# Kernel optimization log

Hardware: AMD Instinct MI355X
Metric: run time of the kernel (lower is better)

The kernel has to match this reference:

```python
import jax, jax.numpy as jnp
import numpy as np

B, C, L = 256, 256, 512
EPS = 1e-5

def setup_inputs() -> dict:
    key = jax.random.key(0)
    k1, k2, k3, k4 = jax.random.split(key, 4)
    x = jax.random.normal(k1, (B, C, L), dtype=jnp.float32)
    idx = jax.random.randint(k2, (B, L), 0, L + 1, dtype=jnp.int32)  # L == pad slot
    # Conv1d(2C, C, 1): weight [C, 2C], bias [C]
    W = jax.random.normal(k3, (C, 2 * C), dtype=jnp.float32) * (1.0 / np.sqrt(2 * C))
    b = jax.random.normal(k4, (C,), dtype=jnp.float32) * 0.01
    return {"x": x, "idx": idx, "W": W, "b": b}

def reference(x, idx, W, b):
    # collect_neighbours: pad length dim with one zero column, gather per (b, l)
    x_pad = jnp.pad(x, ((0, 0), (0, 0), (0, 1)))            # [B, C, L+1]
    nbr = jnp.take_along_axis(x_pad, idx[:, None, :].astype(jnp.int32), axis=2)  # [B, C, L]
    cat = jnp.concatenate([x, nbr], axis=1)                 # [B, 2C, L]
    # 1x1 Conv1d == channel matmul
    y = jnp.einsum('oc,bcl->bol', W, cat) + b[None, :, None]  # [B, C, L]
    # InstanceNorm1d (affine=False): normalize over L per (b, c), biased var
    mu = jnp.mean(y, axis=2, keepdims=True)
    var = jnp.mean(jnp.square(y - mu), axis=2, keepdims=True)
    y = (y - mu) * jax.lax.rsqrt(var + EPS)
    return jax.nn.relu(y)
```

## Files before the change

### kernel.cpp

```cpp
#include <hip/hip_runtime.h>
#include <hip/hip_bf16.h>
#include <stdint.h>

typedef __bf16 bf16x8 __attribute__((ext_vector_type(8)));
typedef float  f32x4  __attribute__((ext_vector_type(4)));

__device__ __forceinline__ uint32_t cvt2(float a, float b) {
    __hip_bfloat162 h = __float22bfloat162_rn(make_float2(a, b));
    uint32_t u; __builtin_memcpy(&u, &h, 4); return u;
}
__device__ __forceinline__ float bflo(uint32_t u) { uint32_t t = u << 16;         float f; __builtin_memcpy(&f, &t, 4); return f; }
__device__ __forceinline__ float bfhi(uint32_t u) { uint32_t t = u & 0xffff0000u; float f; __builtin_memcpy(&f, &t, 4); return f; }
__device__ __forceinline__ int swz(int u) { return u ^ ((u >> 3) & 7); }

__device__ __forceinline__ void gload_lds16(const void* g, void* l) {
    __builtin_amdgcn_global_load_lds(
        (const __attribute__((address_space(1))) uint32_t*)g,
        (__attribute__((address_space(3))) uint32_t*)l,
        16, 0, 0);
}

__global__ __launch_bounds__(256, 4)
void pack_transpose(const float* __restrict__ x, const float* __restrict__ W,
                    unsigned short* __restrict__ xT, unsigned short* __restrict__ wT)
{
    const int tid = threadIdx.x;
    const int id  = blockIdx.x;
    if (id < 2048) {
        const int b  = ((id >> 6) << 3) + (id & 7);
        const int kc = (id >> 3) & 7;
        const int s2 = tid >> 6, l4 = tid & 63;
        const float* src0 = x + ((size_t)b << 17) + ((size_t)((kc << 5) + (s2 << 3)) << 9);
        unsigned short* dst0 = xT + (((size_t)(b << 5) + (kc << 2) + s2) << 12);
        #pragma unroll
        for (int lh = 0; lh < 2; ++lh) {
            const int l0 = (lh << 8) + (l4 << 2);
            f32x4 xr[8];
            #pragma unroll
            for (int j = 0; j < 8; ++j)
                xr[j] = __builtin_nontemporal_load((const f32x4*)(src0 + (j << 9) + l0));
            #pragma unroll
            for (int lv = 0; lv < 4; ++lv) {
                uint4 p;
                p.x = cvt2(xr[0][lv], xr[1][lv]);
                p.y = cvt2(xr[2][lv], xr[3][lv]);
                p.z = cvt2(xr[4][lv], xr[5][lv]);
                p.w = cvt2(xr[6][lv], xr[7][lv]);
                *(uint4*)(dst0 + ((l0 + lv) << 3)) = p;
            }
        }
    } else {
        const int og = id - 2048;
        const int r = tid & 63, sg = tid >> 6;
        const float* wrow = W + ((size_t)((og << 5) + (r & 31)) << 9) + ((r >> 5) << 8);
        #pragma unroll
        for (int ss = 0; ss < 8; ++ss) {
            const int s = (sg << 3) + ss;
            float4 f0 = *(const float4*)(wrow + (s << 3));
            float4 f1 = *(const float4*)(wrow + (s << 3) + 4);
            uint4 p;
            p.x = cvt2(f0.x, f0.y); p.y = cvt2(f0.z, f0.w);
            p.z = cvt2(f1.x, f1.y); p.w = cvt2(f1.z, f1.w);
            *(uint4*)(wT + (((((og << 5) + s) << 6) + r) << 3)) = p;
        }
    }
}

__global__ __launch_bounds__(256, 2)
void edge_gemm(const unsigned short* __restrict__ xT,
               const unsigned short* __restrict__ wT,
               const int* __restrict__ idx,
               float* __restrict__ out)
{
    __shared__ __align__(16) unsigned char smem[73728];
    unsigned short* y2 = (unsigned short*)smem;
    float* red         = (float*)(smem + 36864);

    const int tid  = threadIdx.x;
    const int wv   = tid >> 6;
    const int lane = tid & 63;
    const int m    = lane & 15;
    const int q    = lane >> 4;

    const int id  = blockIdx.x;
    const int rem = id & 63;
    const int b   = ((id >> 6) << 3) + (rem & 7);
    const int og  = rem >> 3;
    const int o0  = og << 5;

    const char* xb = (const char*)xT + ((size_t)b << 18);
    const char* wb = (const char*)wT + (og << 15);

    const int offS = (wv << 10) + (lane << 4);

    int iv[8];
    #pragma unroll
    for (int nt = 0; nt < 8; ++nt)
        iv[nt] = idx[((size_t)b << 9) + (wv << 7) + (nt << 4) + m];

    f32x4 acc[4][8];
    #pragma unroll
    for (int mt = 0; mt < 4; ++mt)
        #pragma unroll
        for (int nt = 0; nt < 8; ++nt)
            acc[mt][nt] = (f32x4){0.f, 0.f, 0.f, 0.f};

    {
        char* Bl = (char*)smem;
        #pragma unroll
        for (int i = 0; i < 8; ++i)
            gload_lds16(xb + (i << 12) + offS, Bl + (i << 12) + offS);
        gload_lds16(wb + offS, Bl + 32768 + offS);
    }
    __syncthreads();

    #pragma unroll
    for (int kc = 0; kc < 8; ++kc) {
        const int cur = kc & 1;
        if (kc < 7) {
            char* Bl = (char*)smem + (cur ^ 1) * 36864;
            const char* Bg = xb + ((kc + 1) << 15);
            #pragma unroll
            for (int i = 0; i < 8; ++i)
                gload_lds16(Bg + (i << 12) + offS, Bl + (i << 12) + offS);
            gload_lds16(wb + ((kc + 1) << 12) + offS, Bl + 32768 + offS);
        }

        const unsigned short* B0 = (const unsigned short*)(smem + cur * 36864);
        const unsigned short* A0 = B0 + 16384;
        bf16x8 av[4], bv[8];
        #pragma unroll
        for (int mt = 0; mt < 4; ++mt)
            av[mt] = *(const bf16x8*)(A0 + (q << 9) + (((mt << 4) + m) << 3));
        #pragma unroll
        for (int nt = 0; nt < 8; ++nt)
            bv[nt] = *(const bf16x8*)(B0 + (q << 12) + (((wv << 7) + (nt << 4) + m) << 3));
        #pragma unroll
        for (int mt = 0; mt < 4; ++mt)
            #pragma unroll
            for (int nt = 0; nt < 8; ++nt)
                acc[mt][nt] = __builtin_amdgcn_mfma_f32_16x16x32_bf16(av[mt], bv[nt], acc[mt][nt], 0, 0, 0);

        if (kc < 7) __syncthreads();
    }

    #pragma unroll
    for (int mt = 2; mt < 4; ++mt)
        #pragma unroll
        for (int nt = 0; nt < 8; ++nt) {
            int col  = (wv << 7) + (nt << 4) + m;
            int row0 = ((mt - 2) << 4) + (q << 2);
            uint2 p;
            p.x = cvt2(acc[mt][nt][0], acc[mt][nt][1]);
            p.y = cvt2(acc[mt][nt][2], acc[mt][nt][3]);
            *(uint2*)(y2 + col * 36 + row0) = p;
        }
    __syncthreads();

    float vvl[2][8][4];
    float s_[2][4], q_[2][4];
    #pragma unroll
    for (int mt = 0; mt < 2; ++mt)
        #pragma unroll
        for (int r4 = 0; r4 < 4; ++r4) { s_[mt][r4] = 0.f; q_[mt][r4] = 0.f; }

    #pragma unroll
    for (int nt = 0; nt < 8; ++nt) {
        int  c   = iv[nt];
        bool inb = (c < 512);
        int  cc  = inb ? c : 0;
        #pragma unroll
        for (int mt = 0; mt < 2; ++mt) {
            uint2 g = *(const uint2*)(y2 + cc * 36 + (mt << 4) + (q << 2));
            float gv[4];
            gv[0] = inb ? bflo(g.x) : 0.f;
            gv[1] = inb ? bfhi(g.x) : 0.f;
            gv[2] = inb ? bflo(g.y) : 0.f;
            gv[3] = inb ? bfhi(g.y) : 0.f;
            #pragma unroll
            for (int r4 = 0; r4 < 4; ++r4) {
                float val = acc[mt][nt][r4] + gv[r4];
                vvl[mt][nt][r4] = val;
                s_[mt][r4] += val;
                q_[mt][r4] += val * val;
            }
        }
    }

    #pragma unroll
    for (int mt = 0; mt < 2; ++mt)
        #pragma unroll
        for (int r4 = 0; r4 < 4; ++r4) {
            float s = s_[mt][r4], ss = q_[mt][r4];
            #pragma unroll
            for (int off = 1; off < 16; off <<= 1) {
                s  += __shfl_xor(s,  off, 64);
                ss += __shfl_xor(ss, off, 64);
            }
            if (m == 0) {
                int r = (mt << 4) + (q << 2) + r4;
                red[(r << 3) + (wv << 1)]     = s;
                red[(r << 3) + (wv << 1) + 1] = ss;
            }
        }
    __syncthreads();

    #pragma unroll
    for (int mt = 0; mt < 2; ++mt)
        #pragma unroll
        for (int r4 = 0; r4 < 4; ++r4) {
            int r = (mt << 4) + (q << 2) + r4;
            float S = red[(r << 3)]     + red[(r << 3) + 2] + red[(r << 3) + 4] + red[(r << 3) + 6];
            float Q = red[(r << 3) + 1] + red[(r << 3) + 3] + red[(r << 3) + 5] + red[(r << 3) + 7];
            float mu  = S * (1.0f / 512.0f);
            float var = Q * (1.0f / 512.0f) - mu * mu;
            float rs  = rsqrtf(var + 1e-5f);
            float* op = out + (((size_t)(b << 8) + o0 + r) << 9) + (wv << 7) + m;
            #pragma unroll
            for (int nt = 0; nt < 8; ++nt) {
                float t = (vvl[mt][nt][r4] - mu) * rs;
                __builtin_nontemporal_store(fmaxf(t, 0.0f), op + (nt << 4));
            }
        }
}

__global__ __launch_bounds__(256, 2)
void edgeconv_fused(const float* __restrict__ x,
                    const int*   __restrict__ idx,
                    const float* __restrict__ W,
                    float*       __restrict__ out)
{
    __shared__ __align__(16) unsigned char smem[65536];
    unsigned short* wlds = (unsigned short*)smem;
    unsigned short* xTl  = (unsigned short*)(smem + 32768);
    unsigned short* y2   = (unsigned short*)smem;
    float*          red  = (float*)(smem + 38912);

    const int tid  = threadIdx.x;
    const int wv   = tid >> 6;
    const int lane = tid & 63;
    const int m    = lane & 15;
    const int q    = lane >> 4;

    const int id  = blockIdx.x;
    const int rem = id & 63;
    const int b   = ((id >> 6) << 3) + (rem & 7);
    const int o0  = (rem >> 3) << 5;

    const float* xb = x + ((size_t)b << 17);

    #pragma unroll
    for (int i = 0; i < 16; ++i) {
        int r = (i << 2) + wv;
        const float4 f = *(const float4*)(W + ((size_t)(o0 + (r & 31)) << 9)
                                            + ((r >> 5) << 8) + (lane << 2));
        uint2 p; p.x = cvt2(f.x, f.y); p.y = cvt2(f.z, f.w);
        int sl = lane >> 1;
        *(uint2*)(wlds + (sl << 9) + ((swz(r) ^ (sl & 7)) << 3) + ((lane & 1) << 2)) = p;
    }

    f32x4 acc[4][8];
    #pragma unroll
    for (int mt = 0; mt < 4; ++mt)
        #pragma unroll
        for (int nt = 0; nt < 8; ++nt)
            acc[mt][nt] = (f32x4){0.f, 0.f, 0.f, 0.f};

    float4 xr0[8], xr1[8];
    auto loadg = [&](int kc, int g, float4* xr) {
        int gid = (g << 8) + tid;
        int s2  = gid >> 7;
        int l4  = gid & 127;
        const float* base = xb + ((size_t)((kc << 5) + (s2 << 3)) << 9) + (l4 << 2);
        #pragma unroll
        for (int j = 0; j < 8; ++j) xr[j] = *(const float4*)(base + (j << 9));
    };
    auto storeg = [&](int g, const float4* xr) {
        int gid = (g << 8) + tid;
        int s2  = gid >> 7;
        int l4  = gid & 127;
        #pragma unroll
        for (int lv = 0; lv < 4; ++lv) {
            int l = (l4 << 2) + lv;
            uint4 p;
            p.x = cvt2((&xr[0].x)[lv], (&xr[1].x)[lv]);
            p.y = cvt2((&xr[2].x)[lv], (&xr[3].x)[lv]);
            p.z = cvt2((&xr[4].x)[lv], (&xr[5].x)[lv]);
            p.w = cvt2((&xr[6].x)[lv], (&xr[7].x)[lv]);
            *(uint4*)(xTl + (s2 << 12) + (swz(l) << 3)) = p;
        }
    };

    loadg(0, 0, xr0);
    loadg(0, 1, xr1);
    storeg(0, xr0);
    storeg(1, xr1);
    __syncthreads();

    for (int kc = 0; kc < 8; ++kc) {
        if (kc < 7) loadg(kc + 1, 0, xr0);

        bf16x8 av[4], bv[8];
        #pragma unroll
        for (int mt = 0; mt < 4; ++mt) {
            int sl = (kc << 2) + q;
            av[mt] = *(const bf16x8*)(wlds + (sl << 9) + ((swz((mt << 4) + m) ^ (sl & 7)) << 3));
        }
        #pragma unroll
        for (int nt = 0; nt < 8; ++nt)
            bv[nt] = *(const bf16x8*)(xTl + (q << 12) + (swz((wv << 7) + (nt << 4) + m) << 3));

        #pragma unroll
        for (int mt = 0; mt < 4; ++mt)
            #pragma unroll
            for (int nt = 0; nt < 8; ++nt)
                acc[mt][nt] = __builtin_amdgcn_mfma_f32_16x16x32_bf16(av[mt], bv[nt], acc[mt][nt], 0, 0, 0);

        if (kc < 7) loadg(kc + 1, 1, xr1);
        __syncthreads();
        if (kc < 7) {
            storeg(0, xr0);
            storeg(1, xr1);
            __syncthreads();
        }
    }

    int iv[8];
    #pragma unroll
    for (int nt = 0; nt < 8; ++nt)
        iv[nt] = idx[((size_t)b << 9) + (wv << 7) + (nt << 4) + m];

    #pragma unroll
    for (int mt = 2; mt < 4; ++mt)
        #pragma unroll
        for (int nt = 0; nt < 8; ++nt) {
            int col  = (wv << 7) + (nt << 4) + m;
            int row0 = ((mt - 2) << 4) + (q << 2);
            uint2 p;
            p.x = cvt2(acc[mt][nt][0], acc[mt][nt][1]);
            p.y = cvt2(acc[mt][nt][2], acc[mt][nt][3]);
            *(uint2*)(y2 + col * 36 + row0) = p;
        }
    __syncthreads();

    float vvl[2][8][4];
    float s_[2][4], q_[2][4];
    #pragma unroll
    for (int mt = 0; mt < 2; ++mt)
        #pragma unroll
        for (int r4 = 0; r4 < 4; ++r4) { s_[mt][r4] = 0.f; q_[mt][r4] = 0.f; }

    #pragma unroll
    for (int nt = 0; nt < 8; ++nt) {
        int  c   = iv[nt];
        bool inb = (c < 512);
        int  cc  = inb ? c : 0;
        #pragma unroll
        for (int mt = 0; mt < 2; ++mt) {
            uint2 g = *(const uint2*)(y2 + cc * 36 + (mt << 4) + (q << 2));
            float gv[4];
            gv[0] = inb ? bflo(g.x) : 0.f;
            gv[1] = inb ? bfhi(g.x) : 0.f;
            gv[2] = inb ? bflo(g.y) : 0.f;
            gv[3] = inb ? bfhi(g.y) : 0.f;
            #pragma unroll
            for (int r4 = 0; r4 < 4; ++r4) {
                float val = acc[mt][nt][r4] + gv[r4];
                vvl[mt][nt][r4] = val;
                s_[mt][r4] += val;
                q_[mt][r4] += val * val;
            }
        }
    }

    #pragma unroll
    for (int mt = 0; mt < 2; ++mt)
        #pragma unroll
        for (int r4 = 0; r4 < 4; ++r4) {
            float s = s_[mt][r4], ss = q_[mt][r4];
            #pragma unroll
            for (int off = 1; off < 16; off <<= 1) {
                s  += __shfl_xor(s,  off, 64);
                ss += __shfl_xor(ss, off, 64);
            }
            if (m == 0) {
                int r = (mt << 4) + (q << 2) + r4;
                red[(r << 3) + (wv << 1)]     = s;
                red[(r << 3) + (wv << 1) + 1] = ss;
            }
        }
    __syncthreads();

    #pragma unroll
    for (int mt = 0; mt < 2; ++mt)
        #pragma unroll
        for (int r4 = 0; r4 < 4; ++r4) {
            int r = (mt << 4) + (q << 2) + r4;
            float S = red[(r << 3)]     + red[(r << 3) + 2] + red[(r << 3) + 4] + red[(r << 3) + 6];
            float Q = red[(r << 3) + 1] + red[(r << 3) + 3] + red[(r << 3) + 5] + red[(r << 3) + 7];
            float mu  = S * (1.0f / 512.0f);
            float var = Q * (1.0f / 512.0f) - mu * mu;
            float rs  = rsqrtf(var + 1e-5f);
            float* op = out + (((size_t)(b << 8) + o0 + r) << 9) + (wv << 7) + m;
            #pragma unroll
            for (int nt = 0; nt < 8; ++nt) {
                float t = (vvl[mt][nt][r4] - mu) * rs;
                op[nt << 4] = fmaxf(t, 0.0f);
            }
        }
}

extern "C" void kernel_launch(void* const* d_in, const int* in_sizes, int n_in,
                              void* d_out, int out_size, void* d_ws, size_t ws_size,
                              hipStream_t stream) {
    const float* x   = (const float*)d_in[0];
    const int*   idx = (const int*)  d_in[1];
    const float* W   = (const float*)d_in[2];
    float* out = (float*)d_out;

    const size_t xT_bytes = (size_t)256 * 32 * 512 * 8 * 2;
    const size_t wT_bytes = (size_t)8 * 32 * 64 * 8 * 2;

    if (ws_size >= xT_bytes + wT_bytes) {
        unsigned short* xT = (unsigned short*)d_ws;
        unsigned short* wT = (unsigned short*)((char*)d_ws + xT_bytes);
        pack_transpose<<<dim3(2056), dim3(256), 0, stream>>>(x, W, xT, wT);
        edge_gemm<<<dim3(2048), dim3(256), 0, stream>>>(xT, wT, idx, out);
    } else {
        edgeconv_fused<<<dim3(2048), dim3(256), 0, stream>>>(x, idx, W, out);
    }
}
```

Baseline: 287.8 us.

## Deepen GEMM prefetch to two stages with vmcnt waits and pad LDS tile

The edge_gemm K-loop now keeps two chunks of global-to-LDS loads in flight. It issues two stages up front, waits with partial s_waitcnt vmcnt counts and raw s_barrier instead of a full __syncthreads, and refills the buffer just consumed. The intent is to hide global load latency behind the MFMA work. The y2 transpose tile moves to its own region with a row stride of 38 instead of 36 to cut LDS bank conflicts, at the cost of more LDS per block and 8-byte accesses that are no longer 8-byte aligned. pack_transpose also issues all 16 vector loads before converting, to raise memory-level parallelism at the cost of more registers.

```diff
diff --git a/kernel.cpp b/kernel.cpp
--- a/kernel.cpp
+++ b/kernel.cpp
@@ -32,20 +32,24 @@
         const int s2 = tid >> 6, l4 = tid & 63;
         const float* src0 = x + ((size_t)b << 17) + ((size_t)((kc << 5) + (s2 << 3)) << 9);
         unsigned short* dst0 = xT + (((size_t)(b << 5) + (kc << 2) + s2) << 12);
+        f32x4 xr[16];
         #pragma unroll
         for (int lh = 0; lh < 2; ++lh) {
             const int l0 = (lh << 8) + (l4 << 2);
-            f32x4 xr[8];
             #pragma unroll
             for (int j = 0; j < 8; ++j)
-                xr[j] = __builtin_nontemporal_load((const f32x4*)(src0 + (j << 9) + l0));
+                xr[(lh << 3) + j] = __builtin_nontemporal_load((const f32x4*)(src0 + (j << 9) + l0));
+        }
+        #pragma unroll
+        for (int lh = 0; lh < 2; ++lh) {
+            const int l0 = (lh << 8) + (l4 << 2);
             #pragma unroll
             for (int lv = 0; lv < 4; ++lv) {
                 uint4 p;
-                p.x = cvt2(xr[0][lv], xr[1][lv]);
-                p.y = cvt2(xr[2][lv], xr[3][lv]);
-                p.z = cvt2(xr[4][lv], xr[5][lv]);
-                p.w = cvt2(xr[6][lv], xr[7][lv]);
+                p.x = cvt2(xr[(lh << 3) + 0][lv], xr[(lh << 3) + 1][lv]);
+                p.y = cvt2(xr[(lh << 3) + 2][lv], xr[(lh << 3) + 3][lv]);
+                p.z = cvt2(xr[(lh << 3) + 4][lv], xr[(lh << 3) + 5][lv]);
+                p.w = cvt2(xr[(lh << 3) + 6][lv], xr[(lh << 3) + 7][lv]);
                 *(uint4*)(dst0 + ((l0 + lv) << 3)) = p;
             }
         }
@@ -72,9 +76,9 @@
                const int* __restrict__ idx,
                float* __restrict__ out)
 {
-    __shared__ __align__(16) unsigned char smem[73728];
-    unsigned short* y2 = (unsigned short*)smem;
-    float* red         = (float*)(smem + 36864);
+    __shared__ __align__(16) unsigned char smem[76032];
+    unsigned short* y2 = (unsigned short*)(smem + 36864);
+    float* red         = (float*)(smem + 75776);
 
     const int tid  = threadIdx.x;
     const int wv   = tid >> 6;
@@ -105,28 +109,27 @@
         for (int nt = 0; nt < 8; ++nt)
             acc[mt][nt] = (f32x4){0.f, 0.f, 0.f, 0.f};
 
-    {
-        char* Bl = (char*)smem;
+    auto stage = [&](int c, int bsel) {
+        char* Bl = (char*)smem + bsel * 36864;
+        const char* Bg = xb + ((size_t)c << 15);
         #pragma unroll
         for (int i = 0; i < 8; ++i)
-            gload_lds16(xb + (i << 12) + offS, Bl + (i << 12) + offS);
-        gload_lds16(wb + offS, Bl + 32768 + offS);
-    }
-    __syncthreads();
+            gload_lds16(Bg + (i << 12) + offS, Bl + (i << 12) + offS);
+        gload_lds16(wb + (c << 12) + offS, Bl + 32768 + offS);
+    };
+
+    stage(0, 1);
+    stage(1, 0);
 
     #pragma unroll
     for (int kc = 0; kc < 8; ++kc) {
-        const int cur = kc & 1;
-        if (kc < 7) {
-            char* Bl = (char*)smem + (cur ^ 1) * 36864;
-            const char* Bg = xb + ((kc + 1) << 15);
-            #pragma unroll
-            for (int i = 0; i < 8; ++i)
-                gload_lds16(Bg + (i << 12) + offS, Bl + (i << 12) + offS);
-            gload_lds16(wb + ((kc + 1) << 12) + offS, Bl + 32768 + offS);
-        }
-
-        const unsigned short* B0 = (const unsigned short*)(smem + cur * 36864);
+        const int bsel = (kc + 1) & 1;
+        if (kc < 7) asm volatile("s_waitcnt vmcnt(9)" ::: "memory");
+        else        asm volatile("s_waitcnt vmcnt(0)" ::: "memory");
+        __builtin_amdgcn_s_barrier();
+        __builtin_amdgcn_sched_barrier(0);
+
+        const unsigned short* B0 = (const unsigned short*)((const char*)smem + bsel * 36864);
         const unsigned short* A0 = B0 + 16384;
         bf16x8 av[4], bv[8];
         #pragma unroll
@@ -141,7 +144,12 @@
             for (int nt = 0; nt < 8; ++nt)
                 acc[mt][nt] = __builtin_amdgcn_mfma_f32_16x16x32_bf16(av[mt], bv[nt], acc[mt][nt], 0, 0, 0);
 
-        if (kc < 7) __syncthreads();
+        __builtin_amdgcn_sched_barrier(0);
+        if (kc < 7) {
+            asm volatile("s_waitcnt lgkmcnt(0)" ::: "memory");
+            __builtin_amdgcn_s_barrier();
+            if (kc < 6) stage(kc + 2, bsel);
+        }
     }
 
     #pragma unroll
@@ -153,7 +161,7 @@
             uint2 p;
             p.x = cvt2(acc[mt][nt][0], acc[mt][nt][1]);
             p.y = cvt2(acc[mt][nt][2], acc[mt][nt][3]);
-            *(uint2*)(y2 + col * 36 + row0) = p;
+            *(uint2*)(y2 + col * 38 + row0) = p;
         }
     __syncthreads();
 
@@ -171,7 +179,7 @@
         int  cc  = inb ? c : 0;
         #pragma unroll
         for (int mt = 0; mt < 2; ++mt) {
-            uint2 g = *(const uint2*)(y2 + cc * 36 + (mt << 4) + (q << 2));
+            uint2 g = *(const uint2*)(y2 + cc * 38 + (mt << 4) + (q << 2));
             float gv[4];
             gv[0] = inb ? bflo(g.x) : 0.f;
             gv[1] = inb ? bfhi(g.x) : 0.f;
```

Result: slower. 305.6 us (+6.2%).

## Stage x transpose through double-buffered LDS with async global-to-LDS loads

Applied to the files above, without the earlier changes.

The pack/transpose path for x now copies each 8-channel slab into shared memory using global_load_lds, double-buffered across the four slabs, and then each thread reads strided LDS values to build its packed bf16 output. Before, each thread issued eight nontemporal 16-byte register loads and wrote four 16-byte stores. The aim is to overlap loading the next slab with converting the current one and to get coalesced contiguous 16-byte writes. In exchange it adds 32KB of LDS per block, which can lower occupancy, adds block-wide syncs, and may cause LDS bank conflicts on the strided reads.

```diff
diff --git a/kernel.cpp b/kernel.cpp
--- a/kernel.cpp
+++ b/kernel.cpp
@@ -27,27 +27,40 @@
     const int tid = threadIdx.x;
     const int id  = blockIdx.x;
     if (id < 2048) {
+        __shared__ __align__(16) float lbuf[2][4096];
         const int b  = ((id >> 6) << 3) + (id & 7);
         const int kc = (id >> 3) & 7;
-        const int s2 = tid >> 6, l4 = tid & 63;
-        const float* src0 = x + ((size_t)b << 17) + ((size_t)((kc << 5) + (s2 << 3)) << 9);
-        unsigned short* dst0 = xT + (((size_t)(b << 5) + (kc << 2) + s2) << 12);
-        #pragma unroll
-        for (int lh = 0; lh < 2; ++lh) {
-            const int l0 = (lh << 8) + (l4 << 2);
-            f32x4 xr[8];
-            #pragma unroll
-            for (int j = 0; j < 8; ++j)
-                xr[j] = __builtin_nontemporal_load((const f32x4*)(src0 + (j << 9) + l0));
-            #pragma unroll
-            for (int lv = 0; lv < 4; ++lv) {
+        const float* src    = x  + ((size_t)b << 17) + ((size_t)(kc << 5) << 9);
+        unsigned short* dst = xT + (((size_t)(b << 5) + (kc << 2)) << 12);
+        const int offS = tid << 4;
+
+        auto stage = [&](int s, int buf) {
+            const char* g = (const char*)(src + (s << 12));
+            char* l = (char*)lbuf[buf];
+            #pragma unroll
+            for (int i = 0; i < 4; ++i)
+                gload_lds16(g + (i << 12) + offS, l + (i << 12) + offS);
+        };
+
+        stage(0, 0);
+        __syncthreads();
+        #pragma unroll
+        for (int s = 0; s < 4; ++s) {
+            const int cur = s & 1;
+            if (s < 3) stage(s + 1, cur ^ 1);
+            const float* Lb = lbuf[cur];
+            unsigned short* sd = dst + ((size_t)s << 12);
+            #pragma unroll
+            for (int half = 0; half < 2; ++half) {
+                const int l = (half << 8) + tid;
                 uint4 p;
-                p.x = cvt2(xr[0][lv], xr[1][lv]);
-                p.y = cvt2(xr[2][lv], xr[3][lv]);
-                p.z = cvt2(xr[4][lv], xr[5][lv]);
-                p.w = cvt2(xr[6][lv], xr[7][lv]);
-                *(uint4*)(dst0 + ((l0 + lv) << 3)) = p;
-            }
+                p.x = cvt2(Lb[l       ], Lb[l +  512]);
+                p.y = cvt2(Lb[l + 1024], Lb[l + 1536]);
+                p.z = cvt2(Lb[l + 2048], Lb[l + 2560]);
+                p.w = cvt2(Lb[l + 3072], Lb[l + 3584]);
+                *(uint4*)(sd + (l << 3)) = p;
+            }
+            if (s < 3) __syncthreads();
         }
     } else {
         const int og = id - 2048;
```

After: 287.1 us. No clear change (-0.2%).
